# Optimization experiments

Hardware: AMD Instinct MI355X
Metric: run time of the kernel (lower is better)

## Reference

```python
import jax, jax.numpy as jnp
import numpy as np

B, N_NODES, T_IN = 512, 32, 12
HID, HEADS, OUT_CH, DEG = 64, 8, 9, 8


def setup_inputs() -> dict:
    key = jax.random.key(0)
    ks = jax.random.split(key, 26)
    rn = lambda k, s, sc=0.1: (jax.random.normal(k, s, jnp.float32) * sc)
    E = B * N_NODES * DEG
    src = jax.random.randint(ks[0], (E,), 0, N_NODES, jnp.int32)
    dst = jax.random.randint(ks[1], (E,), 0, N_NODES, jnp.int32)
    off = jnp.repeat(jnp.arange(B, dtype=jnp.int32) * N_NODES, N_NODES * DEG)
    edge_index = jnp.stack([src + off, dst + off])  # block-diagonal batched graph
    x = jax.random.normal(ks[2], (B, N_NODES, T_IN), jnp.float32)
    return {
        "x": x,
        "edge_index": edge_index,
        # gat1: in=T_IN -> HEADS*HID, concat
        "W1": rn(ks[3], (T_IN, HEADS * HID)),
        "a_src1": rn(ks[4], (HEADS, HID)),
        "a_dst1": rn(ks[5], (HEADS, HID)),
        "b1": rn(ks[6], (HEADS * HID,), 0.01),
        # gat2: in=HEADS*HID -> HID, heads=1, mean (concat=False)
        "W2": rn(ks[7], (HEADS * HID, HID), 0.05),
        "a_src2": rn(ks[8], (1, HID)),
        "a_dst2": rn(ks[9], (1, HID)),
        "b2": rn(ks[10], (HID,), 0.01),
        "gamma": jnp.ones((HID,), jnp.float32),
        "beta": jnp.zeros((HID,), jnp.float32),
        # gru1: input_size=N_NODES(=32), hidden=HID
        "Wi1": rn(ks[11], (3 * HID, N_NODES)),
        "Wh1": rn(ks[12], (3 * HID, HID)),
        "bi1": rn(ks[13], (3 * HID,), 0.01),
        "bh1": rn(ks[14], (3 * HID,), 0.01),
        # gru2: input_size=HID, hidden=HID
        "Wi2": rn(ks[15], (3 * HID, HID)),
        "Wh2": rn(ks[16], (3 * HID, HID)),
        "bi2": rn(ks[17], (3 * HID,), 0.01),
        "bh2": rn(ks[18], (3 * HID,), 0.01),
        "Wf": rn(ks[19], (OUT_CH, HID)),
        "bf": rn(ks[20], (OUT_CH,), 0.01),
    }


def _gat_layer(x, src, dst, W, a_s, a_d, b, concat):
    # PyG GATConv (eval mode, self-loops already appended by caller)
    Nn = x.shape[0]
    heads, hc = a_s.shape
    h = (x @ W).reshape(Nn, heads, hc)                 # [N, H, C]
    es = jnp.sum(h * a_s, axis=-1)                     # [N, H]
    ed = jnp.sum(h * a_d, axis=-1)
    e = jax.nn.leaky_relu(es[src] + ed[dst], 0.2)      # [E, H]
    m = jax.ops.segment_max(e, dst, num_segments=Nn)
    p = jnp.exp(e - m[dst])
    s = jax.ops.segment_sum(p, dst, num_segments=Nn)
    alpha = p / (s[dst] + 1e-16)                       # per-dst softmax
    out = jax.ops.segment_sum(h[src] * alpha[:, :, None], dst, num_segments=Nn)
    out = out.reshape(Nn, heads * hc) if concat else out.mean(axis=1)
    return out + b


def _gru(x, Wi, Wh, bi, bh):
    # torch.nn.GRU (batch_first) single layer; x: [B, T, F]
    H = Wh.shape[1]
    xi = x @ Wi.T + bi                                 # [B, T, 3H]
    def step(h, xt):
        gh = h @ Wh.T + bh
        r = jax.nn.sigmoid(xt[:, :H] + gh[:, :H])
        z = jax.nn.sigmoid(xt[:, H:2 * H] + gh[:, H:2 * H])
        n = jnp.tanh(xt[:, 2 * H:] + r * gh[:, 2 * H:])
        hn = (1.0 - z) * n + z * h
        return hn, hn
    h0 = jnp.zeros((x.shape[0], H), x.dtype)
    _, ys = jax.lax.scan(step, h0, jnp.swapaxes(xi, 0, 1))
    return jnp.swapaxes(ys, 0, 1)


def reference(x, edge_index, W1, a_src1, a_dst1, b1, W2, a_src2, a_dst2, b2,
              gamma, beta, Wi1, Wh1, bi1, bh1, Wi2, Wh2, bi2, bh2, Wf, bf):
    Bsz, Nn_, T = x.shape
    Nn = Bsz * Nn_
    xf = x.reshape(Nn, T)                              # dropout is identity in eval
    sl = jnp.arange(Nn, dtype=edge_index.dtype)        # PyG add_self_loops=True
    src = jnp.concatenate([edge_index[0], sl])
    dst = jnp.concatenate([edge_index[1], sl])
    h = jax.nn.elu(_gat_layer(xf, src, dst, W1, a_src1, a_dst1, b1, True))
    h = jax.nn.elu(_gat_layer(h, src, dst, W2, a_src2, a_dst2, b2, False))
    mu = h.mean(-1, keepdims=True)
    var = ((h - mu) ** 2).mean(-1, keepdims=True)
    h = (h - mu) / jnp.sqrt(var + 1e-5) * gamma + beta
    seq = h.reshape(Bsz, Nn_, -1).transpose(0, 2, 1)   # [B, HID(seq), N_NODES(feat)]
    g = _gru(seq, Wi1, Wh1, bi1, bh1)
    g = _gru(g, Wi2, Wh2, bi2, bh2)
    return g[:, -1, :] @ Wf.T + bf                     # [B, OUT_CH]
```

## Files before the change

### kernel.cpp

```cpp
#include <hip/hip_runtime.h>
#include <hip/hip_bf16.h>
#include <stdint.h>

#define BATCH 512
#define NN 32
#define T_IN 12
#define HID 64
#define HEADS 8
#define OUT_CH 9
#define EPB (NN*8)
#define ETOT (EPB+NN)
#define F1 (HEADS*HID)

using u16 = unsigned short;
using u32 = unsigned int;
typedef _Float16 f16;
typedef _Float16 f16x2 __attribute__((ext_vector_type(2)));
typedef u32 v4u __attribute__((ext_vector_type(4)));
typedef float v4f __attribute__((ext_vector_type(4)));

__device__ __forceinline__ float bf2f(u16 u){ return __uint_as_float(((u32)u)<<16); }
__device__ __forceinline__ u16 f2bf(float f){
    u32 x = __float_as_uint(f);
    u32 r = (x + 0x7FFFu + ((x>>16)&1u))>>16;
    return (u16)r;
}
__device__ __forceinline__ u32 packf16(float a, float b){
    f16x2 p; p.x=(f16)a; p.y=(f16)b; return __builtin_bit_cast(u32,p);
}
__device__ __forceinline__ u16 f2h16(float a){ f16 h=(f16)a; return __builtin_bit_cast(u16,h); }
__device__ __forceinline__ float lof(u32 w){ return (float)__builtin_bit_cast(f16x2,w).x; }
__device__ __forceinline__ float hif(u32 w){ return (float)__builtin_bit_cast(f16x2,w).y; }
__device__ __forceinline__ float dot2(u32 a, u32 b, float c){
#if __has_builtin(__builtin_amdgcn_fdot2)
    return __builtin_amdgcn_fdot2(__builtin_bit_cast(f16x2,a), __builtin_bit_cast(f16x2,b), c, false);
#else
    return fmaf(lof(a),lof(b), fmaf(hif(a),hif(b), c));
#endif
}
__device__ __forceinline__ float elu1(float x){ return x > 0.f ? x : (__expf(x)-1.f); }
__device__ __forceinline__ float sigm(float x){ return 1.f/(1.f+__expf(-x)); }
__device__ __forceinline__ float tanh_(float x){ return 1.f - 2.f/(__expf(2.f*x)+1.f); }
__device__ __forceinline__ u32 fenc(float v){
    u32 b=__float_as_uint(v);
    return (b&0x80000000u) ? ~b : (b|0x80000000u);
}
__device__ __forceinline__ float fdec(u32 k){
    return __uint_as_float((k&0x80000000u) ? (k&0x7FFFFFFFu) : ~k);
}

#define DOT4(acc,A,W) do{ acc=dot2(A.x,W.x,acc); acc=dot2(A.y,W.y,acc); \
                          acc=dot2(A.z,W.z,acc); acc=dot2(A.w,W.w,acc); }while(0)

struct CvtDesc {
    const void* src[16];
    void*       dst[16];
    int         n[16];
};

__global__ __launch_bounds__(256) void k_setup(
    const u32* __restrict__ xw, CvtDesc d,
    const void* __restrict__ W2src, u16* __restrict__ W2i,
    const void* __restrict__ Wi1, const void* __restrict__ Wh1,
    const void* __restrict__ Wi2, const void* __restrict__ Wh2,
    u32* __restrict__ wpk, int* __restrict__ flag)
{
    __shared__ int cnt;
    if(threadIdx.x==0) cnt=0;
    __syncthreads();
    int c=0;
    for(int i=threadIdx.x;i<4096;i+=256){
        u32 w=xw[i];
        if(w & 0x7FFFFFFFu){
            u32 el=(w>>7)&0xFFu;
            if(el>=0x90u) c++;
        }
    }
    atomicAdd(&cnt,c);
    __syncthreads();
    const int f = (cnt>256) ? 1 : 0;
    if(blockIdx.x==0 && threadIdx.x==0) *flag=f;

    const int bk=blockIdx.x;
    if(bk<128){
        int seg=bk>>3, sub=bk&7;
        const void* s=d.src[seg];
        float* o=(float*)d.dst[seg];
        int n=d.n[seg];
        for(int i=sub*256+threadIdx.x;i<n;i+=2048)
            o[i] = f ? ((const float*)s)[i] : bf2f(((const u16*)s)[i]);
    } else if(bk<256){
        int i=(bk-128)*256+threadIdx.x;
        int k=i>>6, j=i&63;
        float v = f? ((const float*)W2src)[i] : bf2f(((const u16*)W2src)[i]);
        W2i[ (((size_t)(k>>3)*64 + j)<<3) + (k&7) ] = f2h16(v);
    } else {
        int w=(bk-256)*256+threadIdx.x;
        int m=w/6144;
        int rem=w-m*6144;
        int row=rem>>5, kw=rem&31;
        const void* s=(m==0)?Wi1:(m==1)?Wh1:(m==2)?Wi2:Wh2;
        int K=(m==0)?32:64;
        int k0=2*kw, k1=k0+1;
        float v0=0.f, v1=0.f;
        if(k0<K) v0 = f? ((const float*)s)[row*K+k0] : bf2f(((const u16*)s)[row*K+k0]);
        if(k1<K) v1 = f? ((const float*)s)[row*K+k1] : bf2f(((const u16*)s)[row*K+k1]);
        wpk[w]=packf16(v0,v1);
    }
}

__global__ __launch_bounds__(256,2) void k_fused(
    const float* __restrict__ x, const int* __restrict__ ei,
    const float* __restrict__ W1, const float* __restrict__ a_s, const float* __restrict__ a_d,
    const float* __restrict__ b1,
    const uint4* __restrict__ W2i, const float* __restrict__ a_s2, const float* __restrict__ a_d2,
    const float* __restrict__ b2, const float* __restrict__ gam, const float* __restrict__ bet,
    const u32* __restrict__ wpk,
    const float* __restrict__ bi1, const float* __restrict__ bh1,
    const float* __restrict__ bi2, const float* __restrict__ bh2,
    const float* __restrict__ Wf, const float* __restrict__ bfv,
    void* __restrict__ outp, const int* __restrict__ flag)
{
    const int b = blockIdx.x, t = threadIdx.x;

    __shared__ __align__(16) float s_x[NN][12];
    __shared__ __align__(16) u16 s_h[NN][520];
    __shared__ __align__(16) u32 s_aspk[HEADS*32], s_adpk[HEADS*32];
    __shared__ float s_es[NN][HEADS], s_ed[NN][HEADS];
    __shared__ unsigned char s_src[ETOT], s_dst[ETOT];
    __shared__ float s_al[HEADS][ETOT];
    __shared__ u32 s_mx[NN*HEADS];
    __shared__ float s_sm[NN*HEADS], s_inv[NN*HEADS];
    __shared__ int s_cnt[NN], s_off[NN], s_fil[NN];
    __shared__ short s_lst[ETOT];
    __shared__ float s_h2[NN][HID];
    __shared__ __align__(16) u32 s_x1[64*16];
    __shared__ __align__(16) u32 s_g1[2][32];
    __shared__ __align__(16) u32 s_g2[2][32];
    __shared__ float s_h2f[64];

    for(int i=t;i<NN*T_IN;i+=256) s_x[i/12][i%12] = x[b*NN*T_IN + i];
    s_aspk[t]=packf16(a_s[2*t],a_s[2*t+1]);
    s_adpk[t]=packf16(a_d[2*t],a_d[2*t+1]);
    s_mx[t]=0u; s_sm[t]=0.f;
    if(t<EPB){
        s_src[t] = (unsigned char)(ei[b*EPB+t] - b*NN);
        s_dst[t] = (unsigned char)(ei[(size_t)BATCH*EPB + b*EPB+t] - b*NN);
    }
    if(t<NN){ s_src[EPB+t]=s_dst[EPB+t]=(unsigned char)t; s_cnt[t]=0; s_fil[t]=0; }
    v4f Wa0,Wa1,Wa2,Wb0,Wb1,Wb2;
    Wa0.x=W1[0*F1+t]; Wa0.y=W1[1*F1+t]; Wa0.z=W1[2*F1+t]; Wa0.w=W1[3*F1+t];
    Wa1.x=W1[4*F1+t]; Wa1.y=W1[5*F1+t]; Wa1.z=W1[6*F1+t]; Wa1.w=W1[7*F1+t];
    Wa2.x=W1[8*F1+t]; Wa2.y=W1[9*F1+t]; Wa2.z=W1[10*F1+t]; Wa2.w=W1[11*F1+t];
    Wb0.x=W1[0*F1+t+256]; Wb0.y=W1[1*F1+t+256]; Wb0.z=W1[2*F1+t+256]; Wb0.w=W1[3*F1+t+256];
    Wb1.x=W1[4*F1+t+256]; Wb1.y=W1[5*F1+t+256]; Wb1.z=W1[6*F1+t+256]; Wb1.w=W1[7*F1+t+256];
    Wb2.x=W1[8*F1+t+256]; Wb2.y=W1[9*F1+t+256]; Wb2.z=W1[10*F1+t+256]; Wb2.w=W1[11*F1+t+256];
    __syncthreads();

    for(int n=0;n<NN;n++){
        const float4* xp=(const float4*)s_x[n];
        float4 xa=xp[0], xb=xp[1], xc=xp[2];
        float A=0.f,B=0.f;
        A=fmaf(xa.x,Wa0.x,A); A=fmaf(xa.y,Wa0.y,A); A=fmaf(xa.z,Wa0.z,A); A=fmaf(xa.w,Wa0.w,A);
        A=fmaf(xb.x,Wa1.x,A); A=fmaf(xb.y,Wa1.y,A); A=fmaf(xb.z,Wa1.z,A); A=fmaf(xb.w,Wa1.w,A);
        A=fmaf(xc.x,Wa2.x,A); A=fmaf(xc.y,Wa2.y,A); A=fmaf(xc.z,Wa2.z,A); A=fmaf(xc.w,Wa2.w,A);
        B=fmaf(xa.x,Wb0.x,B); B=fmaf(xa.y,Wb0.y,B); B=fmaf(xa.z,Wb0.z,B); B=fmaf(xa.w,Wb0.w,B);
        B=fmaf(xb.x,Wb1.x,B); B=fmaf(xb.y,Wb1.y,B); B=fmaf(xb.z,Wb1.z,B); B=fmaf(xb.w,Wb1.w,B);
        B=fmaf(xc.x,Wb2.x,B); B=fmaf(xc.y,Wb2.y,B); B=fmaf(xc.z,Wb2.z,B); B=fmaf(xc.w,Wb2.w,B);
        s_h[n][t]=f2h16(A); s_h[n][t+256]=f2h16(B);
    }
    for(int e=t;e<ETOT;e+=256) atomicAdd(&s_cnt[s_dst[e]],1);
    __syncthreads();

    {
        int n=t&31, hd=t>>5;
        const v4u* hp=(const v4u*)((const u16*)s_h[n] + hd*64);
        v4u h0=hp[0],h1=hp[1],h2=hp[2],h3=hp[3],h4=hp[4],h5=hp[5],h6=hp[6],h7=hp[7];
        const v4u* ap=(const v4u*)&s_aspk[hd*32];
        const v4u* dp=(const v4u*)&s_adpk[hd*32];
        float e1=0.f,e2=0.f;
        { v4u w=ap[0]; DOT4(e1,h0,w); w=ap[1]; DOT4(e1,h1,w); w=ap[2]; DOT4(e1,h2,w); w=ap[3]; DOT4(e1,h3,w);
          w=ap[4]; DOT4(e1,h4,w); w=ap[5]; DOT4(e1,h5,w); w=ap[6]; DOT4(e1,h6,w); w=ap[7]; DOT4(e1,h7,w); }
        { v4u w=dp[0]; DOT4(e2,h0,w); w=dp[1]; DOT4(e2,h1,w); w=dp[2]; DOT4(e2,h2,w); w=dp[3]; DOT4(e2,h3,w);
          w=dp[4]; DOT4(e2,h4,w); w=dp[5]; DOT4(e2,h5,w); w=dp[6]; DOT4(e2,h6,w); w=dp[7]; DOT4(e2,h7,w); }
        s_es[n][hd]=e1; s_ed[n][hd]=e2;
    }
    if(t==0){ int o=0; for(int i=0;i<NN;i++){ s_off[i]=o; o+=s_cnt[i]; } }
    __syncthreads();

    for(int e=t;e<ETOT;e+=256){
        int d=s_dst[e]; int p=atomicAdd(&s_fil[d],1); s_lst[s_off[d]+p]=(short)e;
    }
    for(int i=t;i<ETOT*HEADS;i+=256){
        int hd=i/ETOT, e=i-hd*ETOT;
        int sr=s_src[e], d=s_dst[e];
        float v = s_es[sr][hd]+s_ed[d][hd];
        v = v>0.f? v : 0.2f*v;
        s_al[hd][e]=v;
        atomicMax(&s_mx[d*8+hd], fenc(v));
    }
    __syncthreads();

    for(int i=t;i<ETOT*HEADS;i+=256){
        int hd=i/ETOT, e=i-hd*ETOT;
        int d=s_dst[e];
        float p=__expf(s_al[hd][e]-fdec(s_mx[d*8+hd]));
        s_al[hd][e]=p;
        atomicAdd(&s_sm[d*8+hd], p);
    }
    __syncthreads();
    s_inv[t]=1.f/(s_sm[t]+1e-16f);
    __syncthreads();

    u32 res[32];
    const int dA=t&31, hdA=t>>5;
    {
        int o=s_off[dA], cnt=s_cnt[dA];
        float inv=s_inv[dA*8+hdA];
        #pragma unroll
        for(int ch=0;ch<2;ch++){
            v4f a0=0,a1=0,a2=0,a3=0,a4=0,a5=0,a6=0,a7=0;
            for(int i=0;i<cnt;i++){
                int e=s_lst[o+i]; float av=s_al[hdA][e]; int sr=s_src[e];
                const v4u* hp=(const v4u*)((const u16*)s_h[sr] + hdA*64 + ch*32);
                v4u p0=hp[0],p1=hp[1],p2=hp[2],p3=hp[3];
                a0.x=fmaf(av,lof(p0.x),a0.x); a0.y=fmaf(av,hif(p0.x),a0.y);
                a0.z=fmaf(av,lof(p0.y),a0.z); a0.w=fmaf(av,hif(p0.y),a0.w);
                a1.x=fmaf(av,lof(p0.z),a1.x); a1.y=fmaf(av,hif(p0.z),a1.y);
                a1.z=fmaf(av,lof(p0.w),a1.z); a1.w=fmaf(av,hif(p0.w),a1.w);
                a2.x=fmaf(av,lof(p1.x),a2.x); a2.y=fmaf(av,hif(p1.x),a2.y);
                a2.z=fmaf(av,lof(p1.y),a2.z); a2.w=fmaf(av,hif(p1.y),a2.w);
                a3.x=fmaf(av,lof(p1.z),a3.x); a3.y=fmaf(av,hif(p1.z),a3.y);
                a3.z=fmaf(av,lof(p1.w),a3.z); a3.w=fmaf(av,hif(p1.w),a3.w);
                a4.x=fmaf(av,lof(p2.x),a4.x); a4.y=fmaf(av,hif(p2.x),a4.y);
                a4.z=fmaf(av,lof(p2.y),a4.z); a4.w=fmaf(av,hif(p2.y),a4.w);
                a5.x=fmaf(av,lof(p2.z),a5.x); a5.y=fmaf(av,hif(p2.z),a5.y);
                a5.z=fmaf(av,lof(p2.w),a5.z); a5.w=fmaf(av,hif(p2.w),a5.w);
                a6.x=fmaf(av,lof(p3.x),a6.x); a6.y=fmaf(av,hif(p3.x),a6.y);
                a6.z=fmaf(av,lof(p3.y),a6.z); a6.w=fmaf(av,hif(p3.y),a6.w);
                a7.x=fmaf(av,lof(p3.z),a7.x); a7.y=fmaf(av,hif(p3.z),a7.y);
                a7.z=fmaf(av,lof(p3.w),a7.z); a7.w=fmaf(av,hif(p3.w),a7.w);
            }
            const float* bp = b1 + hdA*64 + ch*32;
            u32* rp = res + ch*16;
            rp[0] = packf16(elu1(a0.x*inv+bp[0]),  elu1(a0.y*inv+bp[1]));
            rp[1] = packf16(elu1(a0.z*inv+bp[2]),  elu1(a0.w*inv+bp[3]));
            rp[2] = packf16(elu1(a1.x*inv+bp[4]),  elu1(a1.y*inv+bp[5]));
            rp[3] = packf16(elu1(a1.z*inv+bp[6]),  elu1(a1.w*inv+bp[7]));
            rp[4] = packf16(elu1(a2.x*inv+bp[8]),  elu1(a2.y*inv+bp[9]));
            rp[5] = packf16(elu1(a2.z*inv+bp[10]), elu1(a2.w*inv+bp[11]));
            rp[6] = packf16(elu1(a3.x*inv+bp[12]), elu1(a3.y*inv+bp[13]));
            rp[7] = packf16(elu1(a3.z*inv+bp[14]), elu1(a3.w*inv+bp[15]));
            rp[8] = packf16(elu1(a4.x*inv+bp[16]), elu1(a4.y*inv+bp[17]));
            rp[9] = packf16(elu1(a4.z*inv+bp[18]), elu1(a4.w*inv+bp[19]));
            rp[10]= packf16(elu1(a5.x*inv+bp[20]), elu1(a5.y*inv+bp[21]));
            rp[11]= packf16(elu1(a5.z*inv+bp[22]), elu1(a5.w*inv+bp[23]));
            rp[12]= packf16(elu1(a6.x*inv+bp[24]), elu1(a6.y*inv+bp[25]));
            rp[13]= packf16(elu1(a6.z*inv+bp[26]), elu1(a6.w*inv+bp[27]));
            rp[14]= packf16(elu1(a7.x*inv+bp[28]), elu1(a7.y*inv+bp[29]));
            rp[15]= packf16(elu1(a7.z*inv+bp[30]), elu1(a7.w*inv+bp[31]));
        }
    }
    __syncthreads();
    {
        u32* rw = ((u32*)s_h) + dA*260 + hdA*32;
        #pragma unroll
        for(int i=0;i<32;i++) rw[i]=res[i];
    }
    if(t<NN){ s_fil[t]=0; s_mx[t]=0u; s_sm[t]=0.f; }
    __syncthreads();

    {
        int n0=(t>>5)<<2, j0=(t&31)<<1;
        const u32* r0=((const u32*)s_h)+(n0+0)*260;
        const u32* r1=((const u32*)s_h)+(n0+1)*260;
        const u32* r2=((const u32*)s_h)+(n0+2)*260;
        const u32* r3=((const u32*)s_h)+(n0+3)*260;
        float a00=0,a01=0,a10=0,a11=0,a20=0,a21=0,a30=0,a31=0;
        for(int kb=0;kb<64;kb++){
            uint4 A0=*(const uint4*)&r0[kb*4];
            uint4 A1=*(const uint4*)&r1[kb*4];
            uint4 A2=*(const uint4*)&r2[kb*4];
            uint4 A3=*(const uint4*)&r3[kb*4];
            const uint4* wp=&W2i[kb*64+j0];
            uint4 w0=wp[0], w1=wp[1];
            a00=dot2(A0.x,w0.x,a00); a00=dot2(A0.y,w0.y,a00); a00=dot2(A0.z,w0.z,a00); a00=dot2(A0.w,w0.w,a00);
            a01=dot2(A0.x,w1.x,a01); a01=dot2(A0.y,w1.y,a01); a01=dot2(A0.z,w1.z,a01); a01=dot2(A0.w,w1.w,a01);
            a10=dot2(A1.x,w0.x,a10); a10=dot2(A1.y,w0.y,a10); a10=dot2(A1.z,w0.z,a10); a10=dot2(A1.w,w0.w,a10);
            a11=dot2(A1.x,w1.x,a11); a11=dot2(A1.y,w1.y,a11); a11=dot2(A1.z,w1.z,a11); a11=dot2(A1.w,w1.w,a11);
            a20=dot2(A2.x,w0.x,a20); a20=dot2(A2.y,w0.y,a20); a20=dot2(A2.z,w0.z,a20); a20=dot2(A2.w,w0.w,a20);
            a21=dot2(A2.x,w1.x,a21); a21=dot2(A2.y,w1.y,a21); a21=dot2(A2.z,w1.z,a21); a21=dot2(A2.w,w1.w,a21);
            a30=dot2(A3.x,w0.x,a30); a30=dot2(A3.y,w0.y,a30); a30=dot2(A3.z,w0.z,a30); a30=dot2(A3.w,w0.w,a30);
            a31=dot2(A3.x,w1.x,a31); a31=dot2(A3.y,w1.y,a31); a31=dot2(A3.z,w1.z,a31); a31=dot2(A3.w,w1.w,a31);
        }
        s_h2[n0+0][j0]=a00; s_h2[n0+0][j0+1]=a01;
        s_h2[n0+1][j0]=a10; s_h2[n0+1][j0+1]=a11;
        s_h2[n0+2][j0]=a20; s_h2[n0+2][j0+1]=a21;
        s_h2[n0+3][j0]=a30; s_h2[n0+3][j0+1]=a31;
    }
    __syncthreads();

    {
        int n=t>>3, g=t&7;
        float e1=0,e2=0;
        #pragma unroll
        for(int cc=0; cc<8; cc++){
            float hv = s_h2[n][g*8+cc];
            e1 += hv*a_s2[g*8+cc];
            e2 += hv*a_d2[g*8+cc];
        }
        #pragma unroll
        for(int m=1;m<8;m<<=1){ e1 += __shfl_xor(e1,m,64); e2 += __shfl_xor(e2,m,64); }
        if(g==0){ s_es[n][0]=e1; s_ed[n][0]=e2; }
    }
    __syncthreads();

    for(int e=t;e<ETOT;e+=256){
        int d=s_dst[e];
        float v = s_es[s_src[e]][0] + s_ed[d][0];
        v = v>0.f? v:0.2f*v;
        s_al[0][e]=v;
        atomicMax(&s_mx[d], fenc(v));
    }
    __syncthreads();

    for(int e=t;e<ETOT;e+=256){
        int d=s_dst[e];
        float p=__expf(s_al[0][e]-fdec(s_mx[d]));
        s_al[0][e]=p;
        atomicAdd(&s_sm[d], p);
    }
    __syncthreads();
    if(t<NN) s_inv[t]=1.f/(s_sm[t]+1e-16f);
    __syncthreads();

    {
        int n=t>>3, g=t&7;
        v4f a0=0, a1=0;
        int o=s_off[n], cnt=s_cnt[n];
        float inv=s_inv[n];
        for(int i=0;i<cnt;i++){
            int e=s_lst[o+i]; float a=s_al[0][e]; int sr=s_src[e];
            const float4* hp=(const float4*)&s_h2[sr][g*8];
            float4 v0=hp[0], v1=hp[1];
            a0.x=fmaf(a,v0.x,a0.x); a0.y=fmaf(a,v0.y,a0.y); a0.z=fmaf(a,v0.z,a0.z); a0.w=fmaf(a,v0.w,a0.w);
            a1.x=fmaf(a,v1.x,a1.x); a1.y=fmaf(a,v1.y,a1.y); a1.z=fmaf(a,v1.z,a1.z); a1.w=fmaf(a,v1.w,a1.w);
        }
        const float* bp=b2+g*8;
        float v0=elu1(a0.x*inv+bp[0]), v1=elu1(a0.y*inv+bp[1]);
        float v2=elu1(a0.z*inv+bp[2]), v3=elu1(a0.w*inv+bp[3]);
        float v4=elu1(a1.x*inv+bp[4]), v5=elu1(a1.y*inv+bp[5]);
        float v6=elu1(a1.z*inv+bp[6]), v7=elu1(a1.w*inv+bp[7]);
        float sum=v0+v1+v2+v3+v4+v5+v6+v7;
        float sq=v0*v0+v1*v1+v2*v2+v3*v3+v4*v4+v5*v5+v6*v6+v7*v7;
        #pragma unroll
        for(int m=1;m<8;m<<=1){ sum+=__shfl_xor(sum,m,64); sq+=__shfl_xor(sq,m,64); }
        float mu = sum*(1.f/64.f);
        float var = sq*(1.f/64.f) - mu*mu;
        float rs = rsqrtf(var + 1e-5f);
        u16* xw=(u16*)s_x1;
        int c=g*8;
        xw[(c+0)*NN+n]=f2h16((v0-mu)*rs*gam[c+0]+bet[c+0]);
        xw[(c+1)*NN+n]=f2h16((v1-mu)*rs*gam[c+1]+bet[c+1]);
        xw[(c+2)*NN+n]=f2h16((v2-mu)*rs*gam[c+2]+bet[c+2]);
        xw[(c+3)*NN+n]=f2h16((v3-mu)*rs*gam[c+3]+bet[c+3]);
        xw[(c+4)*NN+n]=f2h16((v4-mu)*rs*gam[c+4]+bet[c+4]);
        xw[(c+5)*NN+n]=f2h16((v5-mu)*rs*gam[c+5]+bet[c+5]);
        xw[(c+6)*NN+n]=f2h16((v6-mu)*rs*gam[c+6]+bet[c+6]);
        xw[(c+7)*NN+n]=f2h16((v7-mu)*rs*gam[c+7]+bet[c+7]);
    }
    if(t<32){ s_g1[0][t]=0u; s_g1[1][t]=0u; s_g2[0][t]=0u; s_g2[1][t]=0u; }
    __syncthreads();

    {
        const int wave=t>>6, lane=t&63;
        const int layer=wave>>1;
        const int ublk=wave&1;
        const int uu=lane&31, s=lane>>5;
        const int u=ublk*32+uu;

        u32 wiR[16],wiZ[16],wiN[16],whR[16],whZ[16],whN[16];
        const u32* wiu = wpk + (size_t)(layer*2+0)*6144;
        const u32* whu = wpk + (size_t)(layer*2+1)*6144;
        if(layer==0){
            #pragma unroll
            for(int k=0;k<8;k++){
                wiR[k]=wiu[u*32+s*8+k];
                wiZ[k]=wiu[(64+u)*32+s*8+k];
                wiN[k]=wiu[(128+u)*32+s*8+k];
            }
            #pragma unroll
            for(int k=0;k<16;k++){
                whR[k]=whu[u*32+s*16+k];
                whZ[k]=whu[(64+u)*32+s*16+k];
                whN[k]=whu[(128+u)*32+s*16+k];
            }
        } else {
            #pragma unroll
            for(int k=0;k<16;k++){
                wiR[k]=wiu[u*32+s*16+k];
                wiZ[k]=wiu[(64+u)*32+s*16+k];
                wiN[k]=wiu[(128+u)*32+s*16+k];
                whR[k]=whu[u*32+s*16+k];
                whZ[k]=whu[(64+u)*32+s*16+k];
                whN[k]=whu[(128+u)*32+s*16+k];
            }
        }
        const float* bi = layer? bi2:bi1;
        const float* bh = layer? bh2:bh1;
        float br=bi[u]+bh[u], bz=bi[64+u]+bh[64+u], bxn=bi[128+u], bhn=bh[128+u];
        float h=0.f;

        for(int it=0; it<=64; ++it){
            const int pb=(it-1)&1, cb=it&1;
            bool act;
            float pr=0.f,pz=0.f,pxn=0.f,phn=0.f;
            if(layer==0){
                act=(it<64);
                if(act){
                    const u32* xp=&s_x1[it*16+s*8];
                    const u32* hp=&s_g1[pb][s*16];
                    #pragma unroll
                    for(int k=0;k<8;k++){ u32 xv=xp[k]; pr=dot2(xv,wiR[k],pr); pz=dot2(xv,wiZ[k],pz); pxn=dot2(xv,wiN[k],pxn); }
                    #pragma unroll
                    for(int k=0;k<16;k++){ u32 hv=hp[k]; pr=dot2(hv,whR[k],pr); pz=dot2(hv,whZ[k],pz); phn=dot2(hv,whN[k],phn); }
                }
            } else {
                act=(it>=1);
                if(act){
                    const u32* xp=&s_g1[pb][s*16];
                    const u32* hp=&s_g2[pb][s*16];
                    #pragma unroll
                    for(int k=0;k<16;k++){
                        u32 xv=xp[k], hv=hp[k];
                        pr=dot2(xv,wiR[k],pr); pz=dot2(xv,wiZ[k],pz); pxn=dot2(xv,wiN[k],pxn);
                        pr=dot2(hv,whR[k],pr); pz=dot2(hv,whZ[k],pz); phn=dot2(hv,whN[k],phn);
                    }
                }
            }
            if(act){
                pr  += __shfl_xor(pr ,32,64);
                pz  += __shfl_xor(pz ,32,64);
                pxn += __shfl_xor(pxn,32,64);
                phn += __shfl_xor(phn,32,64);
                float r=sigm(pr+br), z=sigm(pz+bz);
                float n=tanh_(pxn+bxn + r*(phn+bhn));
                h=(1.f-z)*n + z*h;
                if(s==0){
                    u16 hv=f2h16(h);
                    if(layer==0) ((u16*)s_g1[cb])[u]=hv;
                    else { ((u16*)s_g2[cb])[u]=hv; if(it==64) s_h2f[u]=h; }
                }
            }
            __syncthreads();
        }
    }

    if(t<OUT_CH){
        float acc=bfv[t];
        const float4* wp=(const float4*)(Wf + t*64);
        const float4* hp=(const float4*)s_h2f;
        #pragma unroll
        for(int k=0;k<16;k++){
            float4 w=wp[k], v=hp[k];
            acc += w.x*v.x + w.y*v.y + w.z*v.z + w.w*v.w;
        }
        if(*flag) ((float*)outp)[b*OUT_CH+t]=acc;
        else      ((u16*)outp)[b*OUT_CH+t]=f2bf(acc);
    }
}

extern "C" void kernel_launch(void* const* d_in, const int* in_sizes, int n_in,
                              void* d_out, int out_size, void* d_ws, size_t ws_size,
                              hipStream_t stream)
{
    char* ws=(char*)d_ws;
    int* flag = (int*)ws;
    float* cf = (float*)(ws + 256);
    float* c_x   = cf; cf+=196608;
    float* c_W1  = cf; cf+=6144;
    float* c_as1 = cf; cf+=512;
    float* c_ad1 = cf; cf+=512;
    float* c_b1  = cf; cf+=512;
    float* c_as2 = cf; cf+=64;
    float* c_ad2 = cf; cf+=64;
    float* c_b2  = cf; cf+=64;
    float* c_gam = cf; cf+=64;
    float* c_bet = cf; cf+=64;
    float* c_bi1 = cf; cf+=192;
    float* c_bh1 = cf; cf+=192;
    float* c_bi2 = cf; cf+=192;
    float* c_bh2 = cf; cf+=192;
    float* c_Wf  = cf; cf+=576;
    float* c_bf  = cf; cf+=9;
    uintptr_t p = ((uintptr_t)cf + 255) & ~(uintptr_t)255;
    u16* c_W2i = (u16*)p;
    p = (p + 32768*2 + 255) & ~(uintptr_t)255;
    u32* wpk = (u32*)p;

    const int* ei = (const int*)d_in[1];

    CvtDesc d;
    const int srcIdx[16] = {0,2,3,4,5,7,8,9,10,11,14,15,18,19,20,21};
    void* dsts[16] = {c_x,c_W1,c_as1,c_ad1,c_b1,c_as2,c_ad2,c_b2,c_gam,c_bet,
                      c_bi1,c_bh1,c_bi2,c_bh2,c_Wf,c_bf};
    const int ns[16] = {196608,6144,512,512,512,64,64,64,64,64,
                        192,192,192,192,576,9};
    for(int i=0;i<16;i++){ d.src[i]=d_in[srcIdx[i]]; d.dst[i]=dsts[i]; d.n[i]=ns[i]; }

    k_setup <<<dim3(352),dim3(256),0,stream>>>((const u32*)d_in[0], d,
                                               d_in[6], c_W2i,
                                               d_in[12], d_in[13], d_in[16], d_in[17],
                                               wpk, flag);
    k_fused <<<dim3(BATCH),dim3(256),0,stream>>>(
        c_x, ei, c_W1, c_as1, c_ad1, c_b1,
        (const uint4*)c_W2i, c_as2, c_ad2, c_b2, c_gam, c_bet,
        wpk, c_bi1, c_bh1, c_bi2, c_bh2,
        c_Wf, c_bf, d_out, flag);
}
```

Measured before the change: 219.8 us.

## Double fused kernel block to 512 threads and split GAT work across them

Raises the fused per-graph kernel from 256 to 512 threads. GAT1 projection, aggregation and the W2 matmul now give each thread half the output columns, while the attention-score, GAT2 and GRU phases keep 256 active threads and leave the rest idle. The aim is to cut per-thread serial work and register pressure in the GAT phases so more waves hide latency. The cost is idle threads in the serial GRU recurrence and barriers across twice as many waves. The launch-bounds change also lowers the per-thread register budget.

```diff
diff --git a/kernel.cpp b/kernel.cpp
--- a/kernel.cpp
+++ b/kernel.cpp
@@ -109,7 +109,7 @@
     }
 }
 
-__global__ __launch_bounds__(256,2) void k_fused(
+__global__ __launch_bounds__(512,4) void k_fused(
     const float* __restrict__ x, const int* __restrict__ ei,
     const float* __restrict__ W1, const float* __restrict__ a_s, const float* __restrict__ a_d,
     const float* __restrict__ b1,
@@ -139,40 +139,36 @@
     __shared__ __align__(16) u32 s_g2[2][32];
     __shared__ float s_h2f[64];
 
-    for(int i=t;i<NN*T_IN;i+=256) s_x[i/12][i%12] = x[b*NN*T_IN + i];
-    s_aspk[t]=packf16(a_s[2*t],a_s[2*t+1]);
-    s_adpk[t]=packf16(a_d[2*t],a_d[2*t+1]);
-    s_mx[t]=0u; s_sm[t]=0.f;
+    for(int i=t;i<NN*T_IN;i+=512) s_x[i/12][i%12] = x[b*NN*T_IN + i];
+    if(t<256){
+        s_aspk[t]=packf16(a_s[2*t],a_s[2*t+1]);
+        s_adpk[t]=packf16(a_d[2*t],a_d[2*t+1]);
+        s_mx[t]=0u; s_sm[t]=0.f;
+    }
     if(t<EPB){
         s_src[t] = (unsigned char)(ei[b*EPB+t] - b*NN);
         s_dst[t] = (unsigned char)(ei[(size_t)BATCH*EPB + b*EPB+t] - b*NN);
     }
     if(t<NN){ s_src[EPB+t]=s_dst[EPB+t]=(unsigned char)t; s_cnt[t]=0; s_fil[t]=0; }
-    v4f Wa0,Wa1,Wa2,Wb0,Wb1,Wb2;
-    Wa0.x=W1[0*F1+t]; Wa0.y=W1[1*F1+t]; Wa0.z=W1[2*F1+t]; Wa0.w=W1[3*F1+t];
-    Wa1.x=W1[4*F1+t]; Wa1.y=W1[5*F1+t]; Wa1.z=W1[6*F1+t]; Wa1.w=W1[7*F1+t];
-    Wa2.x=W1[8*F1+t]; Wa2.y=W1[9*F1+t]; Wa2.z=W1[10*F1+t]; Wa2.w=W1[11*F1+t];
-    Wb0.x=W1[0*F1+t+256]; Wb0.y=W1[1*F1+t+256]; Wb0.z=W1[2*F1+t+256]; Wb0.w=W1[3*F1+t+256];
-    Wb1.x=W1[4*F1+t+256]; Wb1.y=W1[5*F1+t+256]; Wb1.z=W1[6*F1+t+256]; Wb1.w=W1[7*F1+t+256];
-    Wb2.x=W1[8*F1+t+256]; Wb2.y=W1[9*F1+t+256]; Wb2.z=W1[10*F1+t+256]; Wb2.w=W1[11*F1+t+256];
+    v4f Wc0,Wc1,Wc2;
+    Wc0.x=W1[0*F1+t]; Wc0.y=W1[1*F1+t]; Wc0.z=W1[2*F1+t]; Wc0.w=W1[3*F1+t];
+    Wc1.x=W1[4*F1+t]; Wc1.y=W1[5*F1+t]; Wc1.z=W1[6*F1+t]; Wc1.w=W1[7*F1+t];
+    Wc2.x=W1[8*F1+t]; Wc2.y=W1[9*F1+t]; Wc2.z=W1[10*F1+t]; Wc2.w=W1[11*F1+t];
     __syncthreads();
 
     for(int n=0;n<NN;n++){
         const float4* xp=(const float4*)s_x[n];
         float4 xa=xp[0], xb=xp[1], xc=xp[2];
-        float A=0.f,B=0.f;
-        A=fmaf(xa.x,Wa0.x,A); A=fmaf(xa.y,Wa0.y,A); A=fmaf(xa.z,Wa0.z,A); A=fmaf(xa.w,Wa0.w,A);
-        A=fmaf(xb.x,Wa1.x,A); A=fmaf(xb.y,Wa1.y,A); A=fmaf(xb.z,Wa1.z,A); A=fmaf(xb.w,Wa1.w,A);
-        A=fmaf(xc.x,Wa2.x,A); A=fmaf(xc.y,Wa2.y,A); A=fmaf(xc.z,Wa2.z,A); A=fmaf(xc.w,Wa2.w,A);
-        B=fmaf(xa.x,Wb0.x,B); B=fmaf(xa.y,Wb0.y,B); B=fmaf(xa.z,Wb0.z,B); B=fmaf(xa.w,Wb0.w,B);
-        B=fmaf(xb.x,Wb1.x,B); B=fmaf(xb.y,Wb1.y,B); B=fmaf(xb.z,Wb1.z,B); B=fmaf(xb.w,Wb1.w,B);
-        B=fmaf(xc.x,Wb2.x,B); B=fmaf(xc.y,Wb2.y,B); B=fmaf(xc.z,Wb2.z,B); B=fmaf(xc.w,Wb2.w,B);
-        s_h[n][t]=f2h16(A); s_h[n][t+256]=f2h16(B);
-    }
-    for(int e=t;e<ETOT;e+=256) atomicAdd(&s_cnt[s_dst[e]],1);
-    __syncthreads();
-
-    {
+        float A=0.f;
+        A=fmaf(xa.x,Wc0.x,A); A=fmaf(xa.y,Wc0.y,A); A=fmaf(xa.z,Wc0.z,A); A=fmaf(xa.w,Wc0.w,A);
+        A=fmaf(xb.x,Wc1.x,A); A=fmaf(xb.y,Wc1.y,A); A=fmaf(xb.z,Wc1.z,A); A=fmaf(xb.w,Wc1.w,A);
+        A=fmaf(xc.x,Wc2.x,A); A=fmaf(xc.y,Wc2.y,A); A=fmaf(xc.z,Wc2.z,A); A=fmaf(xc.w,Wc2.w,A);
+        s_h[n][t]=f2h16(A);
+    }
+    for(int e=t;e<ETOT;e+=512) atomicAdd(&s_cnt[s_dst[e]],1);
+    __syncthreads();
+
+    if(t<256){
         int n=t&31, hd=t>>5;
         const v4u* hp=(const v4u*)((const u16*)s_h[n] + hd*64);
         v4u h0=hp[0],h1=hp[1],h2=hp[2],h3=hp[3],h4=hp[4],h5=hp[5],h6=hp[6],h7=hp[7];
@@ -188,10 +184,10 @@
     if(t==0){ int o=0; for(int i=0;i<NN;i++){ s_off[i]=o; o+=s_cnt[i]; } }
     __syncthreads();
 
-    for(int e=t;e<ETOT;e+=256){
+    for(int e=t;e<ETOT;e+=512){
         int d=s_dst[e]; int p=atomicAdd(&s_fil[d],1); s_lst[s_off[d]+p]=(short)e;
     }
-    for(int i=t;i<ETOT*HEADS;i+=256){
+    for(int i=t;i<ETOT*HEADS;i+=512){
         int hd=i/ETOT, e=i-hd*ETOT;
         int sr=s_src[e], d=s_dst[e];
         float v = s_es[sr][hd]+s_ed[d][hd];
@@ -201,7 +197,7 @@
     }
     __syncthreads();
 
-    for(int i=t;i<ETOT*HEADS;i+=256){
+    for(int i=t;i<ETOT*HEADS;i+=512){
         int hd=i/ETOT, e=i-hd*ETOT;
         int d=s_dst[e];
         float p=__expf(s_al[hd][e]-fdec(s_mx[d*8+hd]));
@@ -209,98 +205,86 @@
         atomicAdd(&s_sm[d*8+hd], p);
     }
     __syncthreads();
-    s_inv[t]=1.f/(s_sm[t]+1e-16f);
-    __syncthreads();
-
-    u32 res[32];
-    const int dA=t&31, hdA=t>>5;
+    if(t<256) s_inv[t]=1.f/(s_sm[t]+1e-16f);
+    __syncthreads();
+
+    u32 res[16];
+    const int dA=t&31, hdA=(t>>5)&7, chA=t>>8;
     {
         int o=s_off[dA], cnt=s_cnt[dA];
         float inv=s_inv[dA*8+hdA];
+        v4f a0=0,a1=0,a2=0,a3=0,a4=0,a5=0,a6=0,a7=0;
+        for(int i=0;i<cnt;i++){
+            int e=s_lst[o+i]; float av=s_al[hdA][e]; int sr=s_src[e];
+            const v4u* hp=(const v4u*)((const u16*)s_h[sr] + hdA*64 + chA*32);
+            v4u p0=hp[0],p1=hp[1],p2=hp[2],p3=hp[3];
+            a0.x=fmaf(av,lof(p0.x),a0.x); a0.y=fmaf(av,hif(p0.x),a0.y);
+            a0.z=fmaf(av,lof(p0.y),a0.z); a0.w=fmaf(av,hif(p0.y),a0.w);
+            a1.x=fmaf(av,lof(p0.z),a1.x); a1.y=fmaf(av,hif(p0.z),a1.y);
+            a1.z=fmaf(av,lof(p0.w),a1.z); a1.w=fmaf(av,hif(p0.w),a1.w);
+            a2.x=fmaf(av,lof(p1.x),a2.x); a2.y=fmaf(av,hif(p1.x),a2.y);
+            a2.z=fmaf(av,lof(p1.y),a2.z); a2.w=fmaf(av,hif(p1.y),a2.w);
+            a3.x=fmaf(av,lof(p1.z),a3.x); a3.y=fmaf(av,hif(p1.z),a3.y);
+            a3.z=fmaf(av,lof(p1.w),a3.z); a3.w=fmaf(av,hif(p1.w),a3.w);
+            a4.x=fmaf(av,lof(p2.x),a4.x); a4.y=fmaf(av,hif(p2.x),a4.y);
+            a4.z=fmaf(av,lof(p2.y),a4.z); a4.w=fmaf(av,hif(p2.y),a4.w);
+            a5.x=fmaf(av,lof(p2.z),a5.x); a5.y=fmaf(av,hif(p2.z),a5.y);
+            a5.z=fmaf(av,lof(p2.w),a5.z); a5.w=fmaf(av,hif(p2.w),a5.w);
+            a6.x=fmaf(av,lof(p3.x),a6.x); a6.y=fmaf(av,hif(p3.x),a6.y);
+            a6.z=fmaf(av,lof(p3.y),a6.z); a6.w=fmaf(av,hif(p3.y),a6.w);
+            a7.x=fmaf(av,lof(p3.z),a7.x); a7.y=fmaf(av,hif(p3.z),a7.y);
+            a7.z=fmaf(av,lof(p3.w),a7.z); a7.w=fmaf(av,hif(p3.w),a7.w);
+        }
+        const float* bp = b1 + hdA*64 + chA*32;
+        res[0] = packf16(elu1(a0.x*inv+bp[0]),  elu1(a0.y*inv+bp[1]));
+        res[1] = packf16(elu1(a0.z*inv+bp[2]),  elu1(a0.w*inv+bp[3]));
+        res[2] = packf16(elu1(a1.x*inv+bp[4]),  elu1(a1.y*inv+bp[5]));
+        res[3] = packf16(elu1(a1.z*inv+bp[6]),  elu1(a1.w*inv+bp[7]));
+        res[4] = packf16(elu1(a2.x*inv+bp[8]),  elu1(a2.y*inv+bp[9]));
+        res[5] = packf16(elu1(a2.z*inv+bp[10]), elu1(a2.w*inv+bp[11]));
+        res[6] = packf16(elu1(a3.x*inv+bp[12]), elu1(a3.y*inv+bp[13]));
+        res[7] = packf16(elu1(a3.z*inv+bp[14]), elu1(a3.w*inv+bp[15]));
+        res[8] = packf16(elu1(a4.x*inv+bp[16]), elu1(a4.y*inv+bp[17]));
+        res[9] = packf16(elu1(a4.z*inv+bp[18]), elu1(a4.w*inv+bp[19]));
+        res[10]= packf16(elu1(a5.x*inv+bp[20]), elu1(a5.y*inv+bp[21]));
+        res[11]= packf16(elu1(a5.z*inv+bp[22]), elu1(a5.w*inv+bp[23]));
+        res[12]= packf16(elu1(a6.x*inv+bp[24]), elu1(a6.y*inv+bp[25]));
+        res[13]= packf16(elu1(a6.z*inv+bp[26]), elu1(a6.w*inv+bp[27]));
+        res[14]= packf16(elu1(a7.x*inv+bp[28]), elu1(a7.y*inv+bp[29]));
+        res[15]= packf16(elu1(a7.z*inv+bp[30]), elu1(a7.w*inv+bp[31]));
+    }
+    __syncthreads();
+    {
+        u32* rw = ((u32*)s_h) + dA*260 + hdA*32 + chA*16;
         #pragma unroll
-        for(int ch=0;ch<2;ch++){
-            v4f a0=0,a1=0,a2=0,a3=0,a4=0,a5=0,a6=0,a7=0;
-            for(int i=0;i<cnt;i++){
-                int e=s_lst[o+i]; float av=s_al[hdA][e]; int sr=s_src[e];
-                const v4u* hp=(const v4u*)((const u16*)s_h[sr] + hdA*64 + ch*32);
-                v4u p0=hp[0],p1=hp[1],p2=hp[2],p3=hp[3];
-                a0.x=fmaf(av,lof(p0.x),a0.x); a0.y=fmaf(av,hif(p0.x),a0.y);
-                a0.z=fmaf(av,lof(p0.y),a0.z); a0.w=fmaf(av,hif(p0.y),a0.w);
-                a1.x=fmaf(av,lof(p0.z),a1.x); a1.y=fmaf(av,hif(p0.z),a1.y);
-                a1.z=fmaf(av,lof(p0.w),a1.z); a1.w=fmaf(av,hif(p0.w),a1.w);
-                a2.x=fmaf(av,lof(p1.x),a2.x); a2.y=fmaf(av,hif(p1.x),a2.y);
-                a2.z=fmaf(av,lof(p1.y),a2.z); a2.w=fmaf(av,hif(p1.y),a2.w);
-                a3.x=fmaf(av,lof(p1.z),a3.x); a3.y=fmaf(av,hif(p1.z),a3.y);
-                a3.z=fmaf(av,lof(p1.w),a3.z); a3.w=fmaf(av,hif(p1.w),a3.w);
-                a4.x=fmaf(av,lof(p2.x),a4.x); a4.y=fmaf(av,hif(p2.x),a4.y);
-                a4.z=fmaf(av,lof(p2.y),a4.z); a4.w=fmaf(av,hif(p2.y),a4.w);
-                a5.x=fmaf(av,lof(p2.z),a5.x); a5.y=fmaf(av,hif(p2.z),a5.y);
-                a5.z=fmaf(av,lof(p2.w),a5.z); a5.w=fmaf(av,hif(p2.w),a5.w);
-                a6.x=fmaf(av,lof(p3.x),a6.x); a6.y=fmaf(av,hif(p3.x),a6.y);
-                a6.z=fmaf(av,lof(p3.y),a6.z); a6.w=fmaf(av,hif(p3.y),a6.w);
-                a7.x=fmaf(av,lof(p3.z),a7.x); a7.y=fmaf(av,hif(p3.z),a7.y);
-                a7.z=fmaf(av,lof(p3.w),a7.z); a7.w=fmaf(av,hif(p3.w),a7.w);
-            }
-            const float* bp = b1 + hdA*64 + ch*32;
-            u32* rp = res + ch*16;
-            rp[0] = packf16(elu1(a0.x*inv+bp[0]),  elu1(a0.y*inv+bp[1]));
-            rp[1] = packf16(elu1(a0.z*inv+bp[2]),  elu1(a0.w*inv+bp[3]));
-            rp[2] = packf16(elu1(a1.x*inv+bp[4]),  elu1(a1.y*inv+bp[5]));
-            rp[3] = packf16(elu1(a1.z*inv+bp[6]),  elu1(a1.w*inv+bp[7]));
-            rp[4] = packf16(elu1(a2.x*inv+bp[8]),  elu1(a2.y*inv+bp[9]));
-            rp[5] = packf16(elu1(a2.z*inv+bp[10]), elu1(a2.w*inv+bp[11]));
-            rp[6] = packf16(elu1(a3.x*inv+bp[12]), elu1(a3.y*inv+bp[13]));
-            rp[7] = packf16(elu1(a3.z*inv+bp[14]), elu1(a3.w*inv+bp[15]));
-            rp[8] = packf16(elu1(a4.x*inv+bp[16]), elu1(a4.y*inv+bp[17]));
-            rp[9] = packf16(elu1(a4.z*inv+bp[18]), elu1(a4.w*inv+bp[19]));
-            rp[10]= packf16(elu1(a5.x*inv+bp[20]), elu1(a5.y*inv+bp[21]));
-            rp[11]= packf16(elu1(a5.z*inv+bp[22]), elu1(a5.w*inv+bp[23]));
-            rp[12]= packf16(elu1(a6.x*inv+bp[24]), elu1(a6.y*inv+bp[25]));
-            rp[13]= packf16(elu1(a6.z*inv+bp[26]), elu1(a6.w*inv+bp[27]));
-            rp[14]= packf16(elu1(a7.x*inv+bp[28]), elu1(a7.y*inv+bp[29]));
-            rp[15]= packf16(elu1(a7.z*inv+bp[30]), elu1(a7.w*inv+bp[31]));
-        }
-    }
-    __syncthreads();
+        for(int i=0;i<16;i++) rw[i]=res[i];
+    }
+    if(t<NN){ s_fil[t]=0; s_mx[t]=0u; s_sm[t]=0.f; }
+    __syncthreads();
+
     {
-        u32* rw = ((u32*)s_h) + dA*260 + hdA*32;
-        #pragma unroll
-        for(int i=0;i<32;i++) rw[i]=res[i];
-    }
-    if(t<NN){ s_fil[t]=0; s_mx[t]=0u; s_sm[t]=0.f; }
-    __syncthreads();
-
-    {
-        int n0=(t>>5)<<2, j0=(t&31)<<1;
+        int n0=(t>>6)<<2, j=t&63;
         const u32* r0=((const u32*)s_h)+(n0+0)*260;
         const u32* r1=((const u32*)s_h)+(n0+1)*260;
         const u32* r2=((const u32*)s_h)+(n0+2)*260;
         const u32* r3=((const u32*)s_h)+(n0+3)*260;
-        float a00=0,a01=0,a10=0,a11=0,a20=0,a21=0,a30=0,a31=0;
+        float a0=0,a1=0,a2=0,a3=0;
         for(int kb=0;kb<64;kb++){
             uint4 A0=*(const uint4*)&r0[kb*4];
             uint4 A1=*(const uint4*)&r1[kb*4];
             uint4 A2=*(const uint4*)&r2[kb*4];
             uint4 A3=*(const uint4*)&r3[kb*4];
-            const uint4* wp=&W2i[kb*64+j0];
-            uint4 w0=wp[0], w1=wp[1];
-            a00=dot2(A0.x,w0.x,a00); a00=dot2(A0.y,w0.y,a00); a00=dot2(A0.z,w0.z,a00); a00=dot2(A0.w,w0.w,a00);
-            a01=dot2(A0.x,w1.x,a01); a01=dot2(A0.y,w1.y,a01); a01=dot2(A0.z,w1.z,a01); a01=dot2(A0.w,w1.w,a01);
-            a10=dot2(A1.x,w0.x,a10); a10=dot2(A1.y,w0.y,a10); a10=dot2(A1.z,w0.z,a10); a10=dot2(A1.w,w0.w,a10);
-            a11=dot2(A1.x,w1.x,a11); a11=dot2(A1.y,w1.y,a11); a11=dot2(A1.z,w1.z,a11); a11=dot2(A1.w,w1.w,a11);
-            a20=dot2(A2.x,w0.x,a20); a20=dot2(A2.y,w0.y,a20); a20=dot2(A2.z,w0.z,a20); a20=dot2(A2.w,w0.w,a20);
-            a21=dot2(A2.x,w1.x,a21); a21=dot2(A2.y,w1.y,a21); a21=dot2(A2.z,w1.z,a21); a21=dot2(A2.w,w1.w,a21);
-            a30=dot2(A3.x,w0.x,a30); a30=dot2(A3.y,w0.y,a30); a30=dot2(A3.z,w0.z,a30); a30=dot2(A3.w,w0.w,a30);
-            a31=dot2(A3.x,w1.x,a31); a31=dot2(A3.y,w1.y,a31); a31=dot2(A3.z,w1.z,a31); a31=dot2(A3.w,w1.w,a31);
-        }
-        s_h2[n0+0][j0]=a00; s_h2[n0+0][j0+1]=a01;
-        s_h2[n0+1][j0]=a10; s_h2[n0+1][j0+1]=a11;
-        s_h2[n0+2][j0]=a20; s_h2[n0+2][j0+1]=a21;
-        s_h2[n0+3][j0]=a30; s_h2[n0+3][j0+1]=a31;
-    }
-    __syncthreads();
-
-    {
+            uint4 w0=W2i[kb*64+j];
+            a0=dot2(A0.x,w0.x,a0); a0=dot2(A0.y,w0.y,a0); a0=dot2(A0.z,w0.z,a0); a0=dot2(A0.w,w0.w,a0);
+            a1=dot2(A1.x,w0.x,a1); a1=dot2(A1.y,w0.y,a1); a1=dot2(A1.z,w0.z,a1); a1=dot2(A1.w,w0.w,a1);
+            a2=dot2(A2.x,w0.x,a2); a2=dot2(A2.y,w0.y,a2); a2=dot2(A2.z,w0.z,a2); a2=dot2(A2.w,w0.w,a2);
+            a3=dot2(A3.x,w0.x,a3); a3=dot2(A3.y,w0.y,a3); a3=dot2(A3.z,w0.z,a3); a3=dot2(A3.w,w0.w,a3);
+        }
+        s_h2[n0+0][j]=a0; s_h2[n0+1][j]=a1; s_h2[n0+2][j]=a2; s_h2[n0+3][j]=a3;
+    }
+    __syncthreads();
+
+    if(t<256){
         int n=t>>3, g=t&7;
         float e1=0,e2=0;
         #pragma unroll
@@ -315,7 +299,7 @@
     }
     __syncthreads();
 
-    for(int e=t;e<ETOT;e+=256){
+    for(int e=t;e<ETOT;e+=512){
         int d=s_dst[e];
         float v = s_es[s_src[e]][0] + s_ed[d][0];
         v = v>0.f? v:0.2f*v;
@@ -324,7 +308,7 @@
     }
     __syncthreads();
 
-    for(int e=t;e<ETOT;e+=256){
+    for(int e=t;e<ETOT;e+=512){
         int d=s_dst[e];
         float p=__expf(s_al[0][e]-fdec(s_mx[d]));
         s_al[0][e]=p;
@@ -334,7 +318,7 @@
     if(t<NN) s_inv[t]=1.f/(s_sm[t]+1e-16f);
     __syncthreads();
 
-    {
+    if(t<256){
         int n=t>>3, g=t&7;
         v4f a0=0, a1=0;
         int o=s_off[n], cnt=s_cnt[n];
@@ -378,63 +362,69 @@
         const int ublk=wave&1;
         const int uu=lane&31, s=lane>>5;
         const int u=ublk*32+uu;
+        const bool gw = (t<256);
 
         u32 wiR[16],wiZ[16],wiN[16],whR[16],whZ[16],whN[16];
-        const u32* wiu = wpk + (size_t)(layer*2+0)*6144;
-        const u32* whu = wpk + (size_t)(layer*2+1)*6144;
-        if(layer==0){
-            #pragma unroll
-            for(int k=0;k<8;k++){
-                wiR[k]=wiu[u*32+s*8+k];
-                wiZ[k]=wiu[(64+u)*32+s*8+k];
-                wiN[k]=wiu[(128+u)*32+s*8+k];
+        float br=0.f,bz=0.f,bxn=0.f,bhn=0.f;
+        if(gw){
+            const u32* wiu = wpk + (size_t)(layer*2+0)*6144;
+            const u32* whu = wpk + (size_t)(layer*2+1)*6144;
+            if(layer==0){
+                #pragma unroll
+                for(int k=0;k<8;k++){
+                    wiR[k]=wiu[u*32+s*8+k];
+                    wiZ[k]=wiu[(64+u)*32+s*8+k];
+                    wiN[k]=wiu[(128+u)*32+s*8+k];
+                }
+                #pragma unroll
+                for(int k=0;k<16;k++){
+                    whR[k]=whu[u*32+s*16+k];
+                    whZ[k]=whu[(64+u)*32+s*16+k];
+                    whN[k]=whu[(128+u)*32+s*16+k];
+                }
+            } else {
+                #pragma unroll
+                for(int k=0;k<16;k++){
+                    wiR[k]=wiu[u*32+s*16+k];
+                    wiZ[k]=wiu[(64+u)*32+s*16+k];
+                    wiN[k]=wiu[(128+u)*32+s*16+k];
+                    whR[k]=whu[u*32+s*16+k];
+                    whZ[k]=whu[(64+u)*32+s*16+k];
+                    whN[k]=whu[(128+u)*32+s*16+k];
+                }
             }
-            #pragma unroll
-            for(int k=0;k<16;k++){
-                whR[k]=whu[u*32+s*16+k];
-                whZ[k]=whu[(64+u)*32+s*16+k];
-                whN[k]=whu[(128+u)*32+s*16+k];
-            }
-        } else {
-            #pragma unroll
-            for(int k=0;k<16;k++){
-                wiR[k]=wiu[u*32+s*16+k];
-                wiZ[k]=wiu[(64+u)*32+s*16+k];
-                wiN[k]=wiu[(128+u)*32+s*16+k];
-                whR[k]=whu[u*32+s*16+k];
-                whZ[k]=whu[(64+u)*32+s*16+k];
-                whN[k]=whu[(128+u)*32+s*16+k];
-            }
-        }
-        const float* bi = layer? bi2:bi1;
-        const float* bh = layer? bh2:bh1;
-        float br=bi[u]+bh[u], bz=bi[64+u]+bh[64+u], bxn=bi[128+u], bhn=bh[128+u];
+            const float* bi = layer? bi2:bi1;
+            const float* bh = layer? bh2:bh1;
+            br=bi[u]+bh[u]; bz=bi[64+u]+bh[64+u]; bxn=bi[128+u]; bhn=bh[128+u];
+        }
         float h=0.f;
 
         for(int it=0; it<=64; ++it){
             const int pb=(it-1)&1, cb=it&1;
-            bool act;
+            bool act=false;
             float pr=0.f,pz=0.f,pxn=0.f,phn=0.f;
-            if(layer==0){
-                act=(it<64);
-                if(act){
-                    const u32* xp=&s_x1[it*16+s*8];
-                    const u32* hp=&s_g1[pb][s*16];
-                    #pragma unroll
-                    for(int k=0;k<8;k++){ u32 xv=xp[k]; pr=dot2(xv,wiR[k],pr); pz=dot2(xv,wiZ[k],pz); pxn=dot2(xv,wiN[k],pxn); }
-                    #pragma unroll
-                    for(int k=0;k<16;k++){ u32 hv=hp[k]; pr=dot2(hv,whR[k],pr); pz=dot2(hv,whZ[k],pz); phn=dot2(hv,whN[k],phn); }
-                }
-            } else {
-                act=(it>=1);
-                if(act){
-                    const u32* xp=&s_g1[pb][s*16];
-                    const u32* hp=&s_g2[pb][s*16];
-                    #pragma unroll
-                    for(int k=0;k<16;k++){
-                        u32 xv=xp[k], hv=hp[k];
-                        pr=dot2(xv,wiR[k],pr); pz=dot2(xv,wiZ[k],pz); pxn=dot2(xv,wiN[k],pxn);
-                        pr=dot2(hv,whR[k],pr); pz=dot2(hv,whZ[k],pz); phn=dot2(hv,whN[k],phn);
+            if(gw){
+                if(layer==0){
+                    act=(it<64);
+                    if(act){
+                        const u32* xp=&s_x1[it*16+s*8];
+                        const u32* hp=&s_g1[pb][s*16];
+                        #pragma unroll
+                        for(int k=0;k<8;k++){ u32 xv=xp[k]; pr=dot2(xv,wiR[k],pr); pz=dot2(xv,wiZ[k],pz); pxn=dot2(xv,wiN[k],pxn); }
+                        #pragma unroll
+                        for(int k=0;k<16;k++){ u32 hv=hp[k]; pr=dot2(hv,whR[k],pr); pz=dot2(hv,whZ[k],pz); phn=dot2(hv,whN[k],phn); }
+                    }
+                } else {
+                    act=(it>=1);
+                    if(act){
+                        const u32* xp=&s_g1[pb][s*16];
+                        const u32* hp=&s_g2[pb][s*16];
+                        #pragma unroll
+                        for(int k=0;k<16;k++){
+                            u32 xv=xp[k], hv=hp[k];
+                            pr=dot2(xv,wiR[k],pr); pz=dot2(xv,wiZ[k],pz); pxn=dot2(xv,wiN[k],pxn);
+                            pr=dot2(hv,whR[k],pr); pz=dot2(hv,whZ[k],pz); phn=dot2(hv,whN[k],phn);
+                        }
                     }
                 }
             }
@@ -512,7 +502,7 @@
                                                d_in[6], c_W2i,
                                                d_in[12], d_in[13], d_in[16], d_in[17],
                                                wpk, flag);
-    k_fused <<<dim3(BATCH),dim3(256),0,stream>>>(
+    k_fused <<<dim3(BATCH),dim3(512),0,stream>>>(
         c_x, ei, c_W1, c_as1, c_ad1, c_b1,
         (const uint4*)c_W2i, c_as2, c_ad2, c_b2, c_gam, c_bet,
         wpk, c_bi1, c_bh1, c_bi2, c_bh2,
```

After: 254.6 us. 15.8% more time.
